# Kernel optimization log

Hardware: AMD Instinct MI355X
Metric: run time of the kernel (lower is better)

Reference implementation:

```python
import jax, jax.numpy as jnp
import numpy as np

H = 16
D_MODEL = 1024
D_K = D_MODEL // H
MAX_REL = 16
REL_VOCAB = 2 * MAX_REL + 1


def _rel_pos_ids(seq_len):
    r = jnp.arange(seq_len)
    dist = r[None, :] - r[:, None]                      # [S,S]
    return jnp.clip(dist, -MAX_REL, MAX_REL) + MAX_REL  # in [0, 2*MAX_REL]


def setup_inputs() -> dict:
    key = jax.random.key(0)
    ks = jax.random.split(key, 16)
    B, S = 2, 2048
    f32 = jnp.float32
    inp = {
        "query": jax.random.normal(ks[0], (B, S, D_MODEL), f32),
        "key": jax.random.normal(ks[1], (B, S, D_MODEL), f32),
        "value": jax.random.normal(ks[2], (B, S, D_MODEL), f32),
        # four nn.Linear(d_model, d_model): W [out,in], b [out]
        "Wq": jax.random.normal(ks[3], (D_MODEL, D_MODEL), f32) * 0.02,
        "bq": jnp.zeros((D_MODEL,), f32),
        "Wk": jax.random.normal(ks[4], (D_MODEL, D_MODEL), f32) * 0.02,
        "bk": jnp.zeros((D_MODEL,), f32),
        "Wv": jax.random.normal(ks[5], (D_MODEL, D_MODEL), f32) * 0.02,
        "bv": jnp.zeros((D_MODEL,), f32),
        "Wo": jax.random.normal(ks[6], (D_MODEL, D_MODEL), f32) * 0.02,
        "bo": jnp.zeros((D_MODEL,), f32),
        # relative-position embedding tables (keys and values)
        "rel_k_table": jax.random.normal(ks[7], (REL_VOCAB, D_K), f32) * 0.02,
        "rel_v_table": jax.random.normal(ks[8], (REL_VOCAB, D_K), f32) * 0.02,
    }
    return inp


def reference(query, key, value, Wq, bq, Wk, bk, Wv, bv, Wo, bo,
              rel_k_table, rel_v_table):
    B, S, E = query.shape
    ids = _rel_pos_ids(S)                    # [S,S] int
    rel_k = rel_k_table[ids]                 # [S,S,d_k]
    rel_v = rel_v_table[ids]                 # [S,S,d_k]

    def proj(x, W, b):
        y = x @ W.T + b                      # [B,S,E]
        return y.reshape(B, S, H, D_K).transpose(0, 2, 1, 3)  # [B,H,S,d_k]

    q = proj(query, Wq, bq)
    k = proj(key, Wk, bk)
    v = proj(value, Wv, bv)

    # NOTE: original has no 1/sqrt(d_k) scaling and ignores mask — faithful.
    logits = jnp.einsum('bhqd,bhkd->bhqk', q, k) \
           + jnp.einsum('bhqd,qkd->bhqk', q, rel_k)
    w = jax.nn.softmax(logits, axis=-1)      # [B,H,S,S]

    x = jnp.einsum('bhqk,bhkd->bhqd', w, v) \
      + jnp.einsum('bhqk,qkd->bhqd', w, rel_v)

    x = x.transpose(0, 2, 1, 3).reshape(B, S, H * D_K)
    return x @ Wo.T + bo
```

## Files before the change

kernel.cpp:

```cpp
#include <hip/hip_runtime.h>
#include <hip/hip_bf16.h>

typedef unsigned short u16;
typedef __attribute__((ext_vector_type(8))) short short8;
typedef __attribute__((ext_vector_type(4))) short short4_t;
typedef __attribute__((ext_vector_type(4))) float f32x4;

#define MFMA16(a, b, c) __builtin_amdgcn_mfma_f32_16x16x32_bf16((a), (b), (c), 0, 0, 0)

#if __has_builtin(__builtin_amdgcn_mfma_f32_16x16x16bf16_1k)
#define MFMAK16(a, b, c) __builtin_amdgcn_mfma_f32_16x16x16bf16_1k((a), (b), (c), 0, 0, 0)
#elif __has_builtin(__builtin_amdgcn_mfma_f32_16x16x16_bf16)
#define MFMAK16(a, b, c) __builtin_amdgcn_mfma_f32_16x16x16_bf16((a), (b), (c), 0, 0, 0)
#else
__device__ __forceinline__ f32x4 mfmak16_asm(short4_t a, short4_t b, f32x4 c) {
  asm("v_mfma_f32_16x16x16_bf16 %0, %1, %2, %0" : "+v"(c) : "v"(a), "v"(b));
  return c;
}
#define MFMAK16(a, b, c) mfmak16_asm((a), (b), (c))
#endif

#define GLOAD_LDS16(gp, lp)                                          \
  __builtin_amdgcn_global_load_lds(                                  \
      (const __attribute__((address_space(1))) void*)(gp),           \
      (__attribute__((address_space(3))) void*)(lp), 16, 0, 0)
#define SBAR() asm volatile("s_barrier" ::: "memory")
#define WAIT_LGKM0() asm volatile("s_waitcnt lgkmcnt(0)" ::: "memory")
#define WAIT_VM0() asm volatile("s_waitcnt vmcnt(0)" ::: "memory")
#define WAIT_VM4() asm volatile("s_waitcnt vmcnt(4)" ::: "memory")

#define LOG2E 1.44269504088896340736f

__device__ __forceinline__ float us2f(u16 u) {
  union { unsigned int i; float f; } c; c.i = ((unsigned int)u) << 16; return c.f;
}
__device__ __forceinline__ u16 f2us(float f) {
  union { float f; unsigned int i; } c; c.f = f;
  return (u16)((c.i + 0x7fffu + ((c.i >> 16) & 1u)) >> 16);
}
__device__ __forceinline__ unsigned int f2us2(float a, float b) {
  union { __hip_bfloat162 h; unsigned int u; } c;
  c.h = __float22bfloat162_rn(float2{a, b});
  return c.u;
}
__device__ __forceinline__ float exp2fast(float x) {
#if __has_builtin(__builtin_amdgcn_exp2f)
  return __builtin_amdgcn_exp2f(x);
#else
  return exp2f(x);
#endif
}

__global__ __launch_bounds__(256) void cvt_all_kernel(
    const float* x0, const float* x1, const float* x2, const float* w0,
    const float* w1, const float* w2, const float* w3, const float* relk,
    u16* y0, u16* y1, u16* y2, u16* z0, u16* z1, u16* z2, u16* z3,
    u16* relkb) {
  const int z = blockIdx.z;
  if (z == 7) {
    const int i = (blockIdx.x * 256 + threadIdx.x) * 8;
    if (i < 4096) {
      if (i < 2112) {
        const float4 a = *(const float4*)(relk + i);
        const float4 b = *(const float4*)(relk + i + 4);
        unsigned int o[4];
        o[0] = f2us2(a.x, a.y); o[1] = f2us2(a.z, a.w);
        o[2] = f2us2(b.x, b.y); o[3] = f2us2(b.z, b.w);
        *(uint4*)(relkb + i) = *(uint4*)o;
      } else {
        uint4 zz = {0u, 0u, 0u, 0u};
        *(uint4*)(relkb + i) = zz;
      }
    }
    return;
  }
  const float* src; u16* dst; int n;
  switch (z) {
    case 0: src = x0; dst = y0; n = 4194304; break;
    case 1: src = x1; dst = y1; n = 4194304; break;
    case 2: src = x2; dst = y2; n = 4194304; break;
    case 3: src = w0; dst = z0; n = 1048576; break;
    case 4: src = w1; dst = z1; n = 1048576; break;
    case 5: src = w2; dst = z2; n = 1048576; break;
    default: src = w3; dst = z3; n = 1048576; break;
  }
  const int i = (blockIdx.x * 256 + threadIdx.x) * 8;
  if (i < n) {
    const float4 a = *(const float4*)(src + i);
    const float4 b = *(const float4*)(src + i + 4);
    unsigned int o[4];
    o[0] = f2us2(a.x, a.y); o[1] = f2us2(a.z, a.w);
    o[2] = f2us2(b.x, b.y); o[3] = f2us2(b.z, b.w);
    *(uint4*)(dst + i) = *(uint4*)o;
  }
}

template <int MODE, typename OUT>
__device__ __forceinline__ void gemm_body(u16* __restrict__ SM,
                                          const u16* __restrict__ X,
                                          const u16* __restrict__ W,
                                          const float* __restrict__ bias,
                                          OUT* __restrict__ Y, int row0, int col0,
                                          float oscale) {
  u16* As = SM;
  u16* Bs = SM + 8192;
  const int tid = threadIdx.x;
  const int lane = tid & 63;
  const int wid = tid >> 6;
  const int wm = wid >> 1, wn = wid & 1;
  const int l15 = lane & 15, l16 = lane >> 4;
  const int lrow = lane >> 3;
  const int lchunk = (lane & 7) ^ lrow;

  f32x4 acc[4][4];
#pragma unroll
  for (int i = 0; i < 4; i++)
#pragma unroll
    for (int j = 0; j < 4; j++) acc[i][j] = (f32x4){0.f, 0.f, 0.f, 0.f};

  for (int k0 = 0; k0 < 1024; k0 += 64) {
#pragma unroll
    for (int i = 0; i < 4; i++) {
      const int rb = wid * 32 + i * 8;
      GLOAD_LDS16(X + (size_t)(row0 + rb + lrow) * 1024 + k0 + lchunk * 8, &As[rb * 64]);
      GLOAD_LDS16(W + (size_t)(col0 + rb + lrow) * 1024 + k0 + lchunk * 8, &Bs[rb * 64]);
    }
    __syncthreads();
#pragma unroll
    for (int kk = 0; kk < 2; kk++) {
      const int ch = kk * 4 + l16;
      short8 af[4], bfr[4];
#pragma unroll
      for (int t = 0; t < 4; t++) {
        const int m = wm * 64 + t * 16 + l15;
        af[t] = *(const short8*)&As[m * 64 + ((ch ^ (m & 7)) * 8)];
        const int n = wn * 64 + t * 16 + l15;
        bfr[t] = *(const short8*)&Bs[n * 64 + ((ch ^ (n & 7)) * 8)];
      }
#pragma unroll
      for (int tm = 0; tm < 4; tm++)
#pragma unroll
        for (int tn = 0; tn < 4; tn++)
          acc[tm][tn] = MFMA16(af[tm], bfr[tn], acc[tm][tn]);
    }
    __syncthreads();
  }

  if (MODE == 0) {
#pragma unroll
    for (int tn = 0; tn < 4; tn++) {
      const int col = col0 + wn * 64 + tn * 16 + l15;
      const float bv = bias[col];
#pragma unroll
      for (int tm = 0; tm < 4; tm++) {
        const int rowb = row0 + wm * 64 + tm * 16 + l16 * 4;
#pragma unroll
        for (int r = 0; r < 4; r++)
          Y[(size_t)(rowb + r) * 1024 + col] = (OUT)(acc[tm][tn][r] + bv);
      }
    }
  } else {
    u16* T = SM;
    const int bb = row0 >> 11;
    const int sbase = row0 & 2047;
#pragma unroll
    for (int pass = 0; pass < 2; pass++) {
      __syncthreads();
      if (wm == pass) {
#pragma unroll
        for (int tn = 0; tn < 4; tn++) {
          const int coll = wn * 64 + tn * 16 + l15;
          const float bv = bias[col0 + coll];
#pragma unroll
          for (int tm = 0; tm < 4; tm++) {
            if (MODE == 1) {
#pragma unroll
              for (int r = 0; r < 4; r++)
                T[(tm * 16 + l16 * 4 + r) * 136 + coll] = f2us((acc[tm][tn][r] + bv) * oscale);
            } else {
              unsigned int o[2];
              o[0] = f2us2(acc[tm][tn][0] + bv, acc[tm][tn][1] + bv);
              o[1] = f2us2(acc[tm][tn][2] + bv, acc[tm][tn][3] + bv);
              *(short4_t*)&T[coll * 72 + tm * 16 + l16 * 4] = *(short4_t*)o;
            }
          }
        }
      }
      __syncthreads();
      if (MODE == 1) {
#pragma unroll
        for (int i = 0; i < 8; i++) {
          const int idx = tid + i * 256;
          const int srow = idx >> 5, c4 = idx & 31;
          const short4_t v = *(const short4_t*)&T[srow * 136 + c4 * 4];
          const int col = col0 + c4 * 4;
          const int hh = col >> 6, dd = col & 63;
          const int s = sbase + pass * 64 + srow;
          *(short4_t*)&((u16*)Y)[(((size_t)(bb * 16 + hh)) * 2048 + s) * 64 + dd] = v;
        }
      } else {
#pragma unroll
        for (int i = 0; i < 4; i++) {
          const int idx = tid + i * 256;
          const int cl = idx >> 3, sc = idx & 7;
          const short8 v = *(const short8*)&T[cl * 72 + sc * 8];
          const int col = col0 + cl;
          const int hh = col >> 6, dd = col & 63;
          const int s = sbase + pass * 64 + sc * 8;
          *(short8*)&((u16*)Y)[(((size_t)(bb * 16 + hh)) * 64 + dd) * 2048 + s] = v;
        }
      }
    }
  }
}

__global__ __launch_bounds__(256) void qkv_kernel(
    const u16* Xq, const u16* Xk, const u16* Xv, const u16* Wq, const u16* Wk,
    const u16* Wv, const float* bq, const float* bk, const float* bv, u16* Yq,
    u16* Yk, u16* Yv) {
  __shared__ __align__(16) u16 SM[16384];
  const int z = blockIdx.z;
  const u16* X = z == 0 ? Xq : (z == 1 ? Xk : Xv);
  const u16* W = z == 0 ? Wq : (z == 1 ? Wk : Wv);
  const float* bi = z == 0 ? bq : (z == 1 ? bk : bv);
  u16* Y = z == 0 ? Yq : (z == 1 ? Yk : Yv);
  if (z == 2)
    gemm_body<2, u16>(SM, X, W, bi, Y, blockIdx.x * 128, blockIdx.y * 128, 1.0f);
  else
    gemm_body<1, u16>(SM, X, W, bi, Y, blockIdx.x * 128, blockIdx.y * 128,
                      z == 0 ? LOG2E : 1.0f);
}

__global__ __launch_bounds__(256) void oproj_kernel(const u16* Xc, const u16* Wo,
                                                    const float* bo, float* out) {
  __shared__ __align__(16) u16 SM[16384];
  gemm_body<0, float>(SM, Xc, Wo, bo, out, blockIdx.x * 128, blockIdx.y * 128, 1.0f);
}

__global__ __launch_bounds__(256, 4) void attn_kernel(
    const u16* __restrict__ Qg, const u16* __restrict__ Kg,
    const u16* __restrict__ Vtg, const u16* __restrict__ relkb,
    const float* __restrict__ relv, u16* __restrict__ ctx) {
  __shared__ __align__(16) u16 KV[16384];
  __shared__ __align__(16) u16 qrelJ[64 * 33];
  __shared__ __align__(16) u16 wsum[64 * 31];

  const int tid = threadIdx.x, lane = tid & 63, wid = tid >> 6;
  const int l15 = lane & 15, l16 = lane >> 4;
  const int bh = blockIdx.x;
  const int b = bh >> 4, h = bh & 15;
  const int q0 = blockIdx.y * 64;
  const u16* Qb = Qg + (size_t)bh * 2048 * 64;
  const u16* Kb = Kg + (size_t)bh * 2048 * 64;
  const u16* Vtb = Vtg + (size_t)bh * 64 * 2048;

  const int lrow = lane >> 3;
  const int lchunk = (lane & 7) ^ lrow;
  const int qw = wid * 16;
  const int kq4 = l16 * 4;
  const int qrow = qw + l15;

#pragma unroll
  for (int i = 0; i < 2; i++) {
    const int rb = qw + i * 8;
    GLOAD_LDS16(Qb + (size_t)(q0 + rb + lrow) * 64 + lchunk * 8, &KV[rb * 64]);
  }
#pragma unroll
  for (int i = 0; i < 2; i++) {
    const int rb = qw + i * 8;
    GLOAD_LDS16(Kb + (size_t)(rb + lrow) * 64 + lchunk * 8, &KV[8192 + rb * 64]);
  }
#pragma unroll
  for (int i = 0; i < 2; i++) {
    const int rb = qw + i * 8;
    GLOAD_LDS16(Vtb + (size_t)(rb + lrow) * 2048 + lchunk * 8, &KV[12288 + rb * 64]);
  }
  for (int idx = tid; idx < 992; idx += 256) ((unsigned int*)wsum)[idx] = 0u;
  WAIT_VM4();
  SBAR();

  short8 aq[2];
  {
    const int m = qw + l15;
    aq[0] = *(const short8*)&KV[m * 64 + ((l16 ^ (m & 7)) * 8)];
    aq[1] = *(const short8*)&KV[m * 64 + (((4 + l16) ^ (m & 7)) * 8)];
  }
  {
    f32x4 qa[3];
#pragma unroll
    for (int nt = 0; nt < 3; nt++) {
      qa[nt] = (f32x4){0.f, 0.f, 0.f, 0.f};
#pragma unroll
      for (int kk = 0; kk < 2; kk++) {
        const short8 bf =
            *(const short8*)(relkb + (nt * 16 + l15) * 64 + kk * 32 + l16 * 8);
        qa[nt] = MFMA16(aq[kk], bf, qa[nt]);
      }
    }
#pragma unroll
    for (int nt = 0; nt < 3; nt++) {
      if (nt < 2 || l15 == 0) {
#pragma unroll
        for (int r = 0; r < 4; r++)
          qrelJ[(qw + kq4 + r) * 33 + nt * 16 + l15] = f2us(qa[nt][r]);
      }
    }
  }
  WAIT_LGKM0();
  const float q0r = us2f(qrelJ[qrow * 33 + 0]);
  const float q32r = us2f(qrelJ[qrow * 33 + 32]);
  SBAR();

  float l_acc = 0.f, wl_acc = 0.f, wr_acc = 0.f;
  f32x4 Oacc[4];
#pragma unroll
  for (int t = 0; t < 4; t++) Oacc[t] = (f32x4){0.f, 0.f, 0.f, 0.f};

  for (int kt = 0; kt < 32; kt++) {
    const int curb = (kt & 1) ? 0 : 8192;
    const int k0 = kt * 64;
    if (kt < 31) {
      const int sb = curb ^ 8192;
      const int k1 = k0 + 64;
#pragma unroll
      for (int i = 0; i < 2; i++) {
        const int rb = qw + i * 8;
        GLOAD_LDS16(Kb + (size_t)(k1 + rb + lrow) * 64 + lchunk * 8, &KV[sb + rb * 64]);
      }
#pragma unroll
      for (int i = 0; i < 2; i++) {
        const int rb = qw + i * 8;
        GLOAD_LDS16(Vtb + (size_t)(rb + lrow) * 2048 + k1 + lchunk * 8,
                    &KV[sb + 4096 + rb * 64]);
      }
      WAIT_VM4();
    } else {
      WAIT_VM0();
    }
    SBAR();

    const u16* __restrict__ Ks = &KV[curb];
    const u16* __restrict__ Vs = &KV[curb + 4096];

    short4_t pf[4];
    if (k0 + 79 <= q0 || k0 >= q0 + 79) {
      const float eb = (k0 < q0) ? q0r : q32r;
      float ts = 0.f;
#pragma unroll
      for (int tn = 0; tn < 4; tn++) {
        f32x4 sac = (f32x4){0.f, 0.f, 0.f, 0.f};
#pragma unroll
        for (int kk = 0; kk < 2; kk++) {
          const int n = tn * 16 + l15;
          const short8 bk = *(const short8*)&Ks[n * 64 + (((kk * 4 + l16) ^ (n & 7)) * 8)];
          sac = MFMA16(bk, aq[kk], sac);
        }
        float p0 = exp2fast(sac[0] + eb), p1 = exp2fast(sac[1] + eb);
        float p2 = exp2fast(sac[2] + eb), p3 = exp2fast(sac[3] + eb);
        ts += (p0 + p1) + (p2 + p3);
        union { unsigned int u[2]; short4_t s; } c;
        c.u[0] = f2us2(p0, p1);
        c.u[1] = f2us2(p2, p3);
        pf[tn] = c.s;
      }
      l_acc += ts;
      if (k0 < q0) wl_acc += ts; else wr_acc += ts;
    } else {
#pragma unroll
      for (int tn = 0; tn < 4; tn++) {
        f32x4 sac = (f32x4){0.f, 0.f, 0.f, 0.f};
#pragma unroll
        for (int kk = 0; kk < 2; kk++) {
          const int n = tn * 16 + l15;
          const short8 bk = *(const short8*)&Ks[n * 64 + (((kk * 4 + l16) ^ (n & 7)) * 8)];
          sac = MFMA16(bk, aq[kk], sac);
        }
        float pv4[4];
#pragma unroll
        for (int r = 0; r < 4; r++) {
          const int kg = k0 + tn * 16 + kq4 + r;
          const int dlt = kg - (q0 + qrow);
          const int jj = (dlt < -16 ? -16 : (dlt > 16 ? 16 : dlt)) + 16;
          const float pv = exp2fast(sac[r] + us2f(qrelJ[qrow * 33 + jj]));
          pv4[r] = pv;
          l_acc += pv;
          if (dlt <= -16) wl_acc += pv;
          else if (dlt >= 16) wr_acc += pv;
          else wsum[qrow * 31 + (dlt + 15)] = f2us(pv);
        }
        union { unsigned int u[2]; short4_t s; } c;
        c.u[0] = f2us2(pv4[0], pv4[1]);
        c.u[1] = f2us2(pv4[2], pv4[3]);
        pf[tn] = c.s;
      }
    }

    __builtin_amdgcn_s_setprio(1);
#pragma unroll
    for (int td = 0; td < 4; td++) {
      const int row = td * 16 + l15;
      const int rs = row & 7;
#pragma unroll
      for (int kk = 0; kk < 4; kk++) {
        const short4_t vf = *(const short4_t*)&Vs[row * 64 +
                                                  (((kk * 2 + (l16 >> 1)) ^ rs) * 8) +
                                                  (l16 & 1) * 4];
        Oacc[td] = MFMAK16(vf, pf[kk], Oacc[td]);
      }
    }
    __builtin_amdgcn_s_setprio(0);

    SBAR();
  }

  l_acc += __shfl_xor(l_acc, 16); l_acc += __shfl_xor(l_acc, 32);
  wl_acc += __shfl_xor(wl_acc, 16); wl_acc += __shfl_xor(wl_acc, 32);
  wr_acc += __shfl_xor(wr_acc, 16); wr_acc += __shfl_xor(wr_acc, 32);
  const float linv = 1.f / l_acc;
  wl_acc *= linv; wr_acc *= linv;

#pragma unroll
  for (int td = 0; td < 4; td++) {
    const f32x4 rv0 = *(const f32x4*)&relv[td * 16 + kq4];
    const f32x4 rv32 = *(const f32x4*)&relv[32 * 64 + td * 16 + kq4];
#pragma unroll
    for (int r = 0; r < 4; r++)
      Oacc[td][r] = Oacc[td][r] * linv + wl_acc * rv0[r] + wr_acc * rv32[r];
  }
  WAIT_LGKM0();
  for (int j = 1; j <= 31; j++) {
    const float wv = us2f(wsum[qrow * 31 + (j - 1)]) * linv;
#pragma unroll
    for (int td = 0; td < 4; td++) {
      const f32x4 rv = *(const f32x4*)&relv[j * 64 + td * 16 + kq4];
#pragma unroll
      for (int r = 0; r < 4; r++) Oacc[td][r] += wv * rv[r];
    }
  }
#pragma unroll
  for (int td = 0; td < 4; td++) {
    unsigned int o[2];
    o[0] = f2us2(Oacc[td][0], Oacc[td][1]);
    o[1] = f2us2(Oacc[td][2], Oacc[td][3]);
    *(short4_t*)&KV[qrow * 72 + td * 16 + kq4] = *(short4_t*)o;
  }
  WAIT_LGKM0();
  SBAR();
#pragma unroll
  for (int i = 0; i < 2; i++) {
    const int idx = tid + i * 256;
    const int q = idx >> 3, sc = idx & 7;
    const short8 v = *(const short8*)&KV[q * 72 + sc * 8];
    *(short8*)&ctx[((size_t)b * 2048 + q0 + q) * 1024 + h * 64 + sc * 8] = v;
  }
}

extern "C" void kernel_launch(void* const* d_in, const int* in_sizes, int n_in,
                              void* d_out, int out_size, void* d_ws, size_t ws_size,
                              hipStream_t stream) {
  u16* qb = (u16*)d_ws;
  u16* kb = qb + 4194304;
  u16* vtb = kb + 4194304;
  u16* ctx = vtb + 4194304;
  u16* Xq = ctx + 4194304;
  u16* Xk = Xq + 4194304;
  u16* Xv = Xk + 4194304;
  u16* Wqb = Xv + 4194304;
  u16* Wkb = Wqb + 1048576;
  u16* Wvb = Wkb + 1048576;
  u16* Wob = Wvb + 1048576;
  u16* relkb = Wob + 1048576;

  const float* bq = (const float*)d_in[4];
  const float* bk = (const float*)d_in[6];
  const float* bv = (const float*)d_in[8];
  const float* bo = (const float*)d_in[10];
  const float* relk = (const float*)d_in[11];
  const float* relv = (const float*)d_in[12];

  dim3 blk(256);
  cvt_all_kernel<<<dim3(2048, 1, 8), blk, 0, stream>>>(
      (const float*)d_in[0], (const float*)d_in[1], (const float*)d_in[2],
      (const float*)d_in[3], (const float*)d_in[5], (const float*)d_in[7],
      (const float*)d_in[9], relk, Xq, Xk, Xv, Wqb, Wkb, Wvb, Wob, relkb);
  qkv_kernel<<<dim3(32, 8, 3), blk, 0, stream>>>(Xq, Xk, Xv, Wqb, Wkb, Wvb, bq,
                                                 bk, bv, qb, kb, vtb);
  attn_kernel<<<dim3(32, 32), blk, 0, stream>>>(qb, kb, vtb, relkb, relv, ctx);
  oproj_kernel<<<dim3(32, 8), blk, 0, stream>>>(ctx, Wob, bo, (float*)d_out);
}
```

Before: 271.3 us.

## Single-buffer K/V tiles, split loop by diagonal region, sum probabilities via MFMA

```diff
diff --git a/kernel.cpp b/kernel.cpp
--- a/kernel.cpp
+++ b/kernel.cpp
@@ -27,7 +27,6 @@
 #define SBAR() asm volatile("s_barrier" ::: "memory")
 #define WAIT_LGKM0() asm volatile("s_waitcnt lgkmcnt(0)" ::: "memory")
 #define WAIT_VM0() asm volatile("s_waitcnt vmcnt(0)" ::: "memory")
-#define WAIT_VM4() asm volatile("s_waitcnt vmcnt(4)" ::: "memory")
 
 #define LOG2E 1.44269504088896340736f
 
@@ -237,11 +236,11 @@
   gemm_body<0, float>(SM, Xc, Wo, bo, out, blockIdx.x * 128, blockIdx.y * 128, 1.0f);
 }
 
-__global__ __launch_bounds__(256, 4) void attn_kernel(
+__global__ __launch_bounds__(256, 6) void attn_kernel(
     const u16* __restrict__ Qg, const u16* __restrict__ Kg,
     const u16* __restrict__ Vtg, const u16* __restrict__ relkb,
     const float* __restrict__ relv, u16* __restrict__ ctx) {
-  __shared__ __align__(16) u16 KV[16384];
+  __shared__ __align__(16) u16 KV[8192];
   __shared__ __align__(16) u16 qrelJ[64 * 33];
   __shared__ __align__(16) u16 wsum[64 * 31];
 
@@ -249,7 +248,8 @@
   const int l15 = lane & 15, l16 = lane >> 4;
   const int bh = blockIdx.x;
   const int b = bh >> 4, h = bh & 15;
-  const int q0 = blockIdx.y * 64;
+  const int by = blockIdx.y;
+  const int q0 = by * 64;
   const u16* Qb = Qg + (size_t)bh * 2048 * 64;
   const u16* Kb = Kg + (size_t)bh * 2048 * 64;
   const u16* Vtb = Vtg + (size_t)bh * 64 * 2048;
@@ -265,19 +265,8 @@
     const int rb = qw + i * 8;
     GLOAD_LDS16(Qb + (size_t)(q0 + rb + lrow) * 64 + lchunk * 8, &KV[rb * 64]);
   }
-#pragma unroll
-  for (int i = 0; i < 2; i++) {
-    const int rb = qw + i * 8;
-    GLOAD_LDS16(Kb + (size_t)(rb + lrow) * 64 + lchunk * 8, &KV[8192 + rb * 64]);
-  }
-#pragma unroll
-  for (int i = 0; i < 2; i++) {
-    const int rb = qw + i * 8;
-    GLOAD_LDS16(Vtb + (size_t)(rb + lrow) * 2048 + lchunk * 8, &KV[12288 + rb * 64]);
-  }
   for (int idx = tid; idx < 992; idx += 256) ((unsigned int*)wsum)[idx] = 0u;
-  WAIT_VM4();
-  SBAR();
+  __syncthreads();
 
   short8 aq[2];
   {
@@ -309,92 +298,45 @@
   WAIT_LGKM0();
   const float q0r = us2f(qrelJ[qrow * 33 + 0]);
   const float q32r = us2f(qrelJ[qrow * 33 + 32]);
-  SBAR();
-
-  float l_acc = 0.f, wl_acc = 0.f, wr_acc = 0.f;
+  const f32x4 ebl = (f32x4){q0r, q0r, q0r, q0r};
+  const f32x4 ebr = (f32x4){q32r, q32r, q32r, q32r};
+  const f32x4 zf = (f32x4){0.f, 0.f, 0.f, 0.f};
+  const short4_t ones4 = (short4_t){(short)0x3F80, (short)0x3F80,
+                                    (short)0x3F80, (short)0x3F80};
+
+  float wl_p = 0.f, wr_p = 0.f;
+  f32x4 SL = zf, SR = zf, SD = zf;
   f32x4 Oacc[4];
 #pragma unroll
-  for (int t = 0; t < 4; t++) Oacc[t] = (f32x4){0.f, 0.f, 0.f, 0.f};
-
-  for (int kt = 0; kt < 32; kt++) {
-    const int curb = (kt & 1) ? 0 : 8192;
-    const int k0 = kt * 64;
-    if (kt < 31) {
-      const int sb = curb ^ 8192;
-      const int k1 = k0 + 64;
-#pragma unroll
-      for (int i = 0; i < 2; i++) {
-        const int rb = qw + i * 8;
-        GLOAD_LDS16(Kb + (size_t)(k1 + rb + lrow) * 64 + lchunk * 8, &KV[sb + rb * 64]);
-      }
-#pragma unroll
-      for (int i = 0; i < 2; i++) {
-        const int rb = qw + i * 8;
-        GLOAD_LDS16(Vtb + (size_t)(rb + lrow) * 2048 + k1 + lchunk * 8,
-                    &KV[sb + 4096 + rb * 64]);
-      }
-      WAIT_VM4();
-    } else {
-      WAIT_VM0();
-    }
+  for (int t = 0; t < 4; t++) Oacc[t] = zf;
+
+  auto stage = [&](int k0c) {
     SBAR();
-
-    const u16* __restrict__ Ks = &KV[curb];
-    const u16* __restrict__ Vs = &KV[curb + 4096];
-
-    short4_t pf[4];
-    if (k0 + 79 <= q0 || k0 >= q0 + 79) {
-      const float eb = (k0 < q0) ? q0r : q32r;
-      float ts = 0.f;
-#pragma unroll
-      for (int tn = 0; tn < 4; tn++) {
-        f32x4 sac = (f32x4){0.f, 0.f, 0.f, 0.f};
-#pragma unroll
-        for (int kk = 0; kk < 2; kk++) {
-          const int n = tn * 16 + l15;
-          const short8 bk = *(const short8*)&Ks[n * 64 + (((kk * 4 + l16) ^ (n & 7)) * 8)];
-          sac = MFMA16(bk, aq[kk], sac);
-        }
-        float p0 = exp2fast(sac[0] + eb), p1 = exp2fast(sac[1] + eb);
-        float p2 = exp2fast(sac[2] + eb), p3 = exp2fast(sac[3] + eb);
-        ts += (p0 + p1) + (p2 + p3);
-        union { unsigned int u[2]; short4_t s; } c;
-        c.u[0] = f2us2(p0, p1);
-        c.u[1] = f2us2(p2, p3);
-        pf[tn] = c.s;
-      }
-      l_acc += ts;
-      if (k0 < q0) wl_acc += ts; else wr_acc += ts;
-    } else {
-#pragma unroll
-      for (int tn = 0; tn < 4; tn++) {
-        f32x4 sac = (f32x4){0.f, 0.f, 0.f, 0.f};
-#pragma unroll
-        for (int kk = 0; kk < 2; kk++) {
-          const int n = tn * 16 + l15;
-          const short8 bk = *(const short8*)&Ks[n * 64 + (((kk * 4 + l16) ^ (n & 7)) * 8)];
-          sac = MFMA16(bk, aq[kk], sac);
-        }
-        float pv4[4];
-#pragma unroll
-        for (int r = 0; r < 4; r++) {
-          const int kg = k0 + tn * 16 + kq4 + r;
-          const int dlt = kg - (q0 + qrow);
-          const int jj = (dlt < -16 ? -16 : (dlt > 16 ? 16 : dlt)) + 16;
-          const float pv = exp2fast(sac[r] + us2f(qrelJ[qrow * 33 + jj]));
-          pv4[r] = pv;
-          l_acc += pv;
-          if (dlt <= -16) wl_acc += pv;
-          else if (dlt >= 16) wr_acc += pv;
-          else wsum[qrow * 31 + (dlt + 15)] = f2us(pv);
-        }
-        union { unsigned int u[2]; short4_t s; } c;
-        c.u[0] = f2us2(pv4[0], pv4[1]);
-        c.u[1] = f2us2(pv4[2], pv4[3]);
-        pf[tn] = c.s;
-      }
-    }
-
+#pragma unroll
+    for (int i = 0; i < 2; i++) {
+      const int rb = qw + i * 8;
+      GLOAD_LDS16(Kb + (size_t)(k0c + rb + lrow) * 64 + lchunk * 8, &KV[rb * 64]);
+    }
+#pragma unroll
+    for (int i = 0; i < 2; i++) {
+      const int rb = qw + i * 8;
+      GLOAD_LDS16(Vtb + (size_t)(rb + lrow) * 2048 + k0c + lchunk * 8,
+                  &KV[4096 + rb * 64]);
+    }
+    WAIT_VM0();
+    SBAR();
+  };
+
+  auto qk = [&](int tn, f32x4 cin) -> f32x4 {
+    const int n = tn * 16 + l15;
+    const short8 bk0 = *(const short8*)&KV[n * 64 + ((l16 ^ (n & 7)) * 8)];
+    const short8 bk1 = *(const short8*)&KV[n * 64 + (((4 + l16) ^ (n & 7)) * 8)];
+    f32x4 s = MFMA16(bk0, aq[0], cin);
+    s = MFMA16(bk1, aq[1], s);
+    return s;
+  };
+
+  auto pvstep = [&](const short4_t* pf) {
     __builtin_amdgcn_s_setprio(1);
 #pragma unroll
     for (int td = 0; td < 4; td++) {
@@ -402,22 +344,72 @@
       const int rs = row & 7;
 #pragma unroll
       for (int kk = 0; kk < 4; kk++) {
-        const short4_t vf = *(const short4_t*)&Vs[row * 64 +
+        const short4_t vf = *(const short4_t*)&KV[4096 + row * 64 +
                                                   (((kk * 2 + (l16 >> 1)) ^ rs) * 8) +
                                                   (l16 & 1) * 4];
         Oacc[td] = MFMAK16(vf, pf[kk], Oacc[td]);
       }
     }
     __builtin_amdgcn_s_setprio(0);
-
-    SBAR();
-  }
-
-  l_acc += __shfl_xor(l_acc, 16); l_acc += __shfl_xor(l_acc, 32);
-  wl_acc += __shfl_xor(wl_acc, 16); wl_acc += __shfl_xor(wl_acc, 32);
-  wr_acc += __shfl_xor(wr_acc, 16); wr_acc += __shfl_xor(wr_acc, 32);
-  const float linv = 1.f / l_acc;
-  wl_acc *= linv; wr_acc *= linv;
+  };
+
+  auto psum = [&](const short4_t* pf, f32x4& S) {
+#pragma unroll
+    for (int kk = 0; kk < 4; kk++) S = MFMAK16(ones4, pf[kk], S);
+  };
+
+  auto offdiag = [&](f32x4 ebv, f32x4& S) {
+    short4_t pf[4];
+#pragma unroll
+    for (int tn = 0; tn < 4; tn++) {
+      const f32x4 sac = qk(tn, ebv);
+      union { unsigned int u[2]; short4_t s; } c;
+      c.u[0] = f2us2(exp2fast(sac[0]), exp2fast(sac[1]));
+      c.u[1] = f2us2(exp2fast(sac[2]), exp2fast(sac[3]));
+      pf[tn] = c.s;
+    }
+    pvstep(pf);
+    psum(pf, S);
+  };
+
+  auto diag = [&](int k0) {
+    short4_t pf[4];
+#pragma unroll
+    for (int tn = 0; tn < 4; tn++) {
+      const f32x4 sac = qk(tn, zf);
+      float pv4[4];
+#pragma unroll
+      for (int r = 0; r < 4; r++) {
+        const int kg = k0 + tn * 16 + kq4 + r;
+        const int dlt = kg - (q0 + qrow);
+        const int jj = (dlt < -16 ? -16 : (dlt > 16 ? 16 : dlt)) + 16;
+        const float p = exp2fast(sac[r] + us2f(qrelJ[qrow * 33 + jj]));
+        pv4[r] = p;
+        if (dlt <= -16) wl_p += p;
+        else if (dlt >= 16) wr_p += p;
+        else wsum[qrow * 31 + (dlt + 15)] = f2us(p);
+      }
+      union { unsigned int u[2]; short4_t s; } c;
+      c.u[0] = f2us2(pv4[0], pv4[1]);
+      c.u[1] = f2us2(pv4[2], pv4[3]);
+      pf[tn] = c.s;
+    }
+    pvstep(pf);
+    psum(pf, SD);
+  };
+
+  const int dlo = (by >= 1) ? by - 1 : 0;
+  const int dhi = (by + 2 <= 32) ? by + 2 : 32;
+  for (int kt = 0; kt < dlo; ++kt) { stage(kt * 64); offdiag(ebl, SL); }
+  for (int kt = dlo; kt < dhi; ++kt) { stage(kt * 64); diag(kt * 64); }
+  for (int kt = dhi; kt < 32; ++kt) { stage(kt * 64); offdiag(ebr, SR); }
+
+  wl_p += __shfl_xor(wl_p, 16); wl_p += __shfl_xor(wl_p, 32);
+  wr_p += __shfl_xor(wr_p, 16); wr_p += __shfl_xor(wr_p, 32);
+  const float l_total = SL[0] + SR[0] + SD[0];
+  const float linv = 1.f / l_total;
+  const float wl = (SL[0] + wl_p) * linv;
+  const float wr = (SR[0] + wr_p) * linv;
 
 #pragma unroll
   for (int td = 0; td < 4; td++) {
@@ -425,7 +417,7 @@
     const f32x4 rv32 = *(const f32x4*)&relv[32 * 64 + td * 16 + kq4];
 #pragma unroll
     for (int r = 0; r < 4; r++)
-      Oacc[td][r] = Oacc[td][r] * linv + wl_acc * rv0[r] + wr_acc * rv32[r];
+      Oacc[td][r] = Oacc[td][r] * linv + wl * rv0[r] + wr * rv32[r];
   }
   WAIT_LGKM0();
   for (int j = 1; j <= 31; j++) {
@@ -437,6 +429,7 @@
       for (int r = 0; r < 4; r++) Oacc[td][r] += wv * rv[r];
     }
   }
+  SBAR();
 #pragma unroll
   for (int td = 0; td < 4; td++) {
     unsigned int o[2];
```

New measurement: 263.2 us. 1.03x faster.
